# Kernel optimization log

Measured on AMD Instinct MI355X. Metric: run time of the kernel, lower is better.

## Reference

```python
import jax, jax.numpy as jnp
import numpy as np

K = 5  # top-k

def setup_inputs() -> dict:
    key = jax.random.key(0)
    k1, k2, k3 = jax.random.split(key, 3)
    B, L, D = 4096, 100000, 256
    predicted_embeddings = jax.random.normal(k1, (B, D), dtype=jnp.float32)
    label_embeddings = jax.random.normal(k2, (L, D), dtype=jnp.float32)
    true_labels = jax.random.randint(k3, (B,), 0, L, dtype=jnp.int64)
    return {
        "predicted_embeddings": predicted_embeddings,
        "label_embeddings": label_embeddings,
        "true_labels": true_labels,
    }

def reference(predicted_embeddings, label_embeddings, true_labels):
    # (B, L) dense similarity
    similarity = jnp.einsum("bd,ld->bl", predicted_embeddings, label_embeddings)
    _, top_k_indices = jax.lax.top_k(similarity, K)  # (B, K)
    correct = jnp.any(top_k_indices == true_labels[:, None], axis=1)
    accuracy = jnp.mean(correct.astype(jnp.float32))
    return accuracy
```

## Files before the change

### kernel.cpp

```cpp
#include <hip/hip_runtime.h>
#include <hip/hip_bf16.h>

#define B_ROWS   4096
#define L_LABELS 100000
#define D_DIM    256
#define TOPK     5
#define SLABN    64
#define NGROUP   8
#define SLABBYTES 32768

#define CUT       4096
#define NSLAB_C   (CUT / SLABN)
#define NG2       ((L_LABELS - CUT) / 16)
#define P2_BLOCKS 256

typedef __bf16 bf16x8 __attribute__((ext_vector_type(8)));
typedef __bf16 bf16x4 __attribute__((ext_vector_type(4)));
typedef float  f32x4  __attribute__((ext_vector_type(4)));

__device__ __forceinline__ void async16(const void* g, void* l) {
    __builtin_amdgcn_global_load_lds(
        (const __attribute__((address_space(1))) unsigned int*)g,
        (__attribute__((address_space(3))) unsigned int*)l,
        16, 0, 0);
}

__global__ void convertL_kernel(const float* __restrict__ src,
                                __hip_bfloat16* __restrict__ dst) {
    size_t i = ((size_t)blockIdx.x * blockDim.x + threadIdx.x) * 8;
    float4 a = *(const float4*)(src + i);
    float4 b = *(const float4*)(src + i + 4);
    bf16x8 v = {(__bf16)a.x, (__bf16)a.y, (__bf16)a.z, (__bf16)a.w,
                (__bf16)b.x, (__bf16)b.y, (__bf16)b.z, (__bf16)b.w};
    *(bf16x8*)((__bf16*)dst + i) = v;
}

__global__ void prep_kernel(const float* __restrict__ P,
                            const float* __restrict__ Lab,
                            const int*   __restrict__ labels,
                            float* __restrict__ s_t,
                            int*   __restrict__ counts,
                            int*   __restrict__ counts2,
                            __hip_bfloat16* __restrict__ Pb,
                            int do_conv) {
    int gwave = (blockIdx.x * blockDim.x + threadIdx.x) >> 6;
    int lane  = threadIdx.x & 63;
    if (gwave >= B_ROWS) return;
    int t = labels[gwave];
    const float4* p4 = (const float4*)(P + (size_t)gwave * D_DIM);
    const float4* l4 = (const float4*)(Lab + (size_t)t * D_DIM);
    float4 a = p4[lane];
    float4 b = l4[lane];
    if (do_conv) {
        bf16x4 pv = {(__bf16)a.x, (__bf16)a.y, (__bf16)a.z, (__bf16)a.w};
        *(bf16x4*)((__bf16*)Pb + (size_t)gwave * D_DIM + lane * 4) = pv;
    }
    float sum = 0.f;
    sum += (float)(__bf16)a.x * (float)(__bf16)b.x;
    sum += (float)(__bf16)a.y * (float)(__bf16)b.y;
    sum += (float)(__bf16)a.z * (float)(__bf16)b.z;
    sum += (float)(__bf16)a.w * (float)(__bf16)b.w;
    #pragma unroll
    for (int m = 1; m < 64; m <<= 1) sum += __shfl_xor(sum, m, 64);
    if (lane == 0) {
        s_t[gwave]     = sum;
        counts[gwave]  = 0;
        counts2[gwave] = 0;
    }
}

#define CBM 64

__global__ __launch_bounds__(512, 4)
void count_kernel_c1(const __hip_bfloat16* __restrict__ Pb,
                     const __hip_bfloat16* __restrict__ Lb,
                     const int*   __restrict__ labels,
                     const float* __restrict__ s_t,
                     int* __restrict__ counts) {
    __shared__ __align__(16) __bf16 Bs[2 * SLABN * D_DIM];

    const int group = blockIdx.x;
    const int Mbase = blockIdx.y * CBM;
    const int tid   = threadIdx.x;
    const int wave  = tid >> 6;
    const int lane  = tid & 63;
    const int wm    = wave >> 2;
    const int wn    = wave & 3;
    const int quad  = lane >> 4;
    const int cc    = lane & 15;

    const int s0 = group * (NSLAB_C / NGROUP);
    const int s1 = s0 + (NSLAB_C / NGROUP);

    const int qc0  = tid & 31;
    const int rw0  = tid >> 5;
    const int gc0  = (qc0 & 24) | ((qc0 ^ rw0) & 7);
    const int dma0 = rw0 * 512 + gc0 * 16;
    const int ldsw = wave * 1024;

    {
        const char* gbase = (const char*)Lb + (size_t)s0 * SLABBYTES;
        #pragma unroll
        for (int j = 0; j < 4; ++j)
            async16(gbase + dma0 + j * 8192,
                    (char*)Bs + ldsw + j * 8192);
    }

    bf16x8 af[2][8];
    #pragma unroll
    for (int mi = 0; mi < 2; ++mi) {
        int row = Mbase + wm * 32 + mi * 16 + cc;
        const __bf16* ap = (const __bf16*)Pb + (size_t)row * D_DIM + quad * 8;
        #pragma unroll
        for (int kb = 0; kb < 8; ++kb)
            af[mi][kb] = *(const bf16x8*)(ap + kb * 32);
    }

    float sr[2][4];
    int   tr[2][4];
    #pragma unroll
    for (int mi = 0; mi < 2; ++mi)
        #pragma unroll
        for (int r = 0; r < 4; ++r) {
            int row = Mbase + wm * 32 + mi * 16 + quad * 4 + r;
            sr[mi][r] = s_t[row];
            tr[mi][r] = labels[row];
        }

    int cnt[2][4] = {};

    for (int s = s0, it = 0; s < s1; ++s, ++it) {
        __syncthreads();

        if (s + 1 < s1) {
            const char* gbase = (const char*)Lb + (size_t)(s + 1) * SLABBYTES;
            char* lbase = (char*)Bs + (size_t)(~it & 1) * SLABBYTES + ldsw;
            #pragma unroll
            for (int j = 0; j < 4; ++j)
                async16(gbase + dma0 + j * 8192, lbase + j * 8192);
        }

        const __bf16* bp = Bs + (size_t)(it & 1) * (SLABN * D_DIM);

        f32x4 acc[2] = {};
        #pragma unroll
        for (int kb = 0; kb < 8; ++kb) {
            int ci = kb * 4 + quad;
            int qc = (ci & 24) | ((ci ^ cc) & 7);
            bf16x8 b = *(const bf16x8*)&bp[(wn * 16 + cc) * D_DIM + qc * 8];
            #pragma unroll
            for (int mi = 0; mi < 2; ++mi)
                acc[mi] = __builtin_amdgcn_mfma_f32_16x16x32_bf16(
                    af[mi][kb], b, acc[mi], 0, 0, 0);
        }

        int n = s * SLABN + wn * 16 + cc;
        #pragma unroll
        for (int mi = 0; mi < 2; ++mi)
            #pragma unroll
            for (int r = 0; r < 4; ++r) {
                float sv = acc[mi][r];
                bool beat = (n != tr[mi][r]) &&
                            (sv > sr[mi][r] ||
                             (sv == sr[mi][r] && n < tr[mi][r]));
                cnt[mi][r] += beat ? 1 : 0;
            }
    }

    #pragma unroll
    for (int mi = 0; mi < 2; ++mi)
        #pragma unroll
        for (int r = 0; r < 4; ++r) {
            int v = cnt[mi][r];
            v += __shfl_xor(v, 1, 64);
            v += __shfl_xor(v, 2, 64);
            v += __shfl_xor(v, 4, 64);
            v += __shfl_xor(v, 8, 64);
            if (cc == 0) {
                int row = Mbase + wm * 32 + mi * 16 + quad * 4 + r;
                atomicAdd(&counts[row], v);
            }
        }
}

__global__ __launch_bounds__(256)
void count_kernel_p2(const __hip_bfloat16* __restrict__ Pb,
                     const float* __restrict__ Lab,
                     const int*   __restrict__ labels,
                     const float* __restrict__ s_t,
                     const int*   __restrict__ counts,
                     int* __restrict__ counts2) {
    __shared__ int cnt_s[B_ROWS];
    __shared__ int surv_s[B_ROWS];
    __shared__ int ns_s;

    const int tid  = threadIdx.x;
    const int wave = tid >> 6;
    const int lane = tid & 63;
    const int quad = lane >> 4;
    const int cc   = lane & 15;

    #pragma unroll
    for (int i = 0; i < B_ROWS / 256; ++i)
        cnt_s[i * 256 + tid] = counts[i * 256 + tid];
    __syncthreads();

    if (wave == 0) {
        int total = 0;
        for (int base = 0; base < B_ROWS; base += 64) {
            bool sv = cnt_s[base + lane] < TOPK;
            unsigned long long m = __ballot(sv);
            int pos = total + __popcll(m & ((1ull << lane) - 1ull));
            if (sv) surv_s[pos] = base + lane;
            total += __popcll(m);
        }
        if (lane == 0) ns_s = total;
    }
    __syncthreads();

    const int ns = ns_s;
    if (ns == 0) return;
    const int ntiles = (ns + 15) >> 4;

    for (int ti = 0; ti < ntiles; ++ti) {
        int arow = surv_s[min(ti * 16 + cc, ns - 1)];
        bf16x8 af2[8];
        const __bf16* ap = (const __bf16*)Pb + (size_t)arow * D_DIM + quad * 8;
        #pragma unroll
        for (int kb = 0; kb < 8; ++kb)
            af2[kb] = *(const bf16x8*)(ap + kb * 32);

        float sr2[4]; int tr2[4], sidx[4];
        #pragma unroll
        for (int r = 0; r < 4; ++r) {
            int rr  = surv_s[min(ti * 16 + quad * 4 + r, ns - 1)];
            sidx[r] = rr;
            sr2[r]  = s_t[rr];
            tr2[r]  = labels[rr];
        }

        int cnt2[4] = {};
        for (int g = blockIdx.x * 4 + wave; g < NG2; g += P2_BLOCKS * 4) {
            int Lbase = CUT + g * 16;
            const float* bb = Lab + (size_t)(Lbase + cc) * D_DIM + quad * 8;
            f32x4 acc = {};
            #pragma unroll
            for (int kb = 0; kb < 8; ++kb) {
                float4 x = *(const float4*)(bb + kb * 32);
                float4 y = *(const float4*)(bb + kb * 32 + 4);
                bf16x8 b = {(__bf16)x.x, (__bf16)x.y, (__bf16)x.z, (__bf16)x.w,
                            (__bf16)y.x, (__bf16)y.y, (__bf16)y.z, (__bf16)y.w};
                acc = __builtin_amdgcn_mfma_f32_16x16x32_bf16(
                    af2[kb], b, acc, 0, 0, 0);
            }
            int n = Lbase + cc;
            #pragma unroll
            for (int r = 0; r < 4; ++r) {
                float sv = acc[r];
                bool beat = (n != tr2[r]) &&
                            (sv > sr2[r] || (sv == sr2[r] && n < tr2[r]));
                cnt2[r] += beat ? 1 : 0;
            }
        }

        #pragma unroll
        for (int r = 0; r < 4; ++r) {
            int v = cnt2[r];
            v += __shfl_xor(v, 1, 64);
            v += __shfl_xor(v, 2, 64);
            v += __shfl_xor(v, 4, 64);
            v += __shfl_xor(v, 8, 64);
            if (cc == 0 && (ti * 16 + quad * 4 + r) < ns && v)
                atomicAdd(&counts2[sidx[r]], v);
        }
    }
}

#define FBM 128
#define FBN 128
#define FBK 32
#define KPAD 40

__global__ __launch_bounds__(256)
void count_kernel_slow(const float* __restrict__ P,
                       const float* __restrict__ Lab,
                       const int*   __restrict__ labels,
                       const float* __restrict__ s_t,
                       int* __restrict__ counts) {
    __shared__ __align__(16) __bf16 As[FBM][KPAD];
    __shared__ __align__(16) __bf16 Bs[FBN][KPAD];

    const int Nbase = blockIdx.x * FBN;
    const int Mbase = blockIdx.y * FBM;
    const int tid  = threadIdx.x;
    const int lane = tid & 63;
    const int wave = tid >> 6;
    const int wm = wave >> 1;
    const int wn = wave & 1;
    const int quad = lane >> 4;
    const int c    = lane & 15;

    const int srow  = tid >> 1;
    const int skoff = (tid & 1) * 16;
    const int brow_g = min(Nbase + srow, L_LABELS - 1);

    f32x4 acc[4][4] = {};

    for (int Kb = 0; Kb < D_DIM; Kb += FBK) {
        const float* gA = P   + (size_t)(Mbase + srow) * D_DIM + Kb + skoff;
        const float* gB = Lab + (size_t)brow_g        * D_DIM + Kb + skoff;
        #pragma unroll
        for (int i = 0; i < 4; ++i) {
            float4 va = *(const float4*)(gA + i * 4);
            float4 vb = *(const float4*)(gB + i * 4);
            *(bf16x4*)&As[srow][skoff + i * 4] =
                (bf16x4){(__bf16)va.x, (__bf16)va.y, (__bf16)va.z, (__bf16)va.w};
            *(bf16x4*)&Bs[srow][skoff + i * 4] =
                (bf16x4){(__bf16)vb.x, (__bf16)vb.y, (__bf16)vb.z, (__bf16)vb.w};
        }
        __syncthreads();

        bf16x8 afr[4], bfr[4];
        #pragma unroll
        for (int mi = 0; mi < 4; ++mi)
            afr[mi] = *(const bf16x8*)&As[wm * 64 + mi * 16 + c][quad * 8];
        #pragma unroll
        for (int ni = 0; ni < 4; ++ni)
            bfr[ni] = *(const bf16x8*)&Bs[wn * 64 + ni * 16 + c][quad * 8];

        #pragma unroll
        for (int mi = 0; mi < 4; ++mi)
            #pragma unroll
            for (int ni = 0; ni < 4; ++ni)
                acc[mi][ni] = __builtin_amdgcn_mfma_f32_16x16x32_bf16(
                    afr[mi], bfr[ni], acc[mi][ni], 0, 0, 0);
        __syncthreads();
    }

    #pragma unroll
    for (int mi = 0; mi < 4; ++mi) {
        int rowb = Mbase + wm * 64 + mi * 16 + quad * 4;
        #pragma unroll
        for (int r = 0; r < 4; ++r) {
            int   row = rowb + r;
            float st  = s_t[row];
            int   t   = labels[row];
            int   cnt = 0;
            #pragma unroll
            for (int ni = 0; ni < 4; ++ni) {
                int   n = Nbase + wn * 64 + ni * 16 + c;
                float s = acc[mi][ni][r];
                bool beat = (n < L_LABELS) && (n != t) &&
                            (s > st || (s == st && n < t));
                cnt += beat ? 1 : 0;
            }
            cnt += __shfl_xor(cnt, 1, 64);
            cnt += __shfl_xor(cnt, 2, 64);
            cnt += __shfl_xor(cnt, 4, 64);
            cnt += __shfl_xor(cnt, 8, 64);
            if (c == 0 && cnt) atomicAdd(&counts[row], cnt);
        }
    }
}

__global__ void finalize_kernel(const int* __restrict__ counts,
                                const int* __restrict__ counts2,
                                float* __restrict__ out) {
    __shared__ int sdata[4];
    int tid = threadIdx.x;
    int local = 0;
    for (int i = tid; i < B_ROWS; i += 256)
        local += (counts[i] + counts2[i] < TOPK) ? 1 : 0;
    #pragma unroll
    for (int m = 1; m < 64; m <<= 1) local += __shfl_xor(local, m, 64);
    if ((tid & 63) == 0) sdata[tid >> 6] = local;
    __syncthreads();
    if (tid == 0)
        out[0] = (float)(sdata[0] + sdata[1] + sdata[2] + sdata[3]) /
                 (float)B_ROWS;
}

extern "C" void kernel_launch(void* const* d_in, const int* in_sizes, int n_in,
                              void* d_out, int out_size, void* d_ws, size_t ws_size,
                              hipStream_t stream) {
    const float* P      = (const float*)d_in[0];
    const float* Lab    = (const float*)d_in[1];
    const int*   labels = (const int*)d_in[2];
    float* out = (float*)d_out;

    float* s_t     = (float*)d_ws;
    int*   counts  = (int*)((char*)d_ws + 16384);
    int*   counts2 = (int*)((char*)d_ws + 32768);

    const size_t pb_off = 49152;
    const size_t lb_off = pb_off + (size_t)B_ROWS * D_DIM * 2;
    const size_t need   = lb_off + (size_t)CUT * D_DIM * 2;

    int fast = (ws_size >= need) ? 1 : 0;
    __hip_bfloat16* Pb = (__hip_bfloat16*)((char*)d_ws + pb_off);
    __hip_bfloat16* Lb = (__hip_bfloat16*)((char*)d_ws + lb_off);

    prep_kernel<<<dim3(B_ROWS / 4), 256, 0, stream>>>(
        P, Lab, labels, s_t, counts, counts2, Pb, fast);

    if (fast) {
        convertL_kernel<<<dim3((CUT * D_DIM) / 2048), 256, 0, stream>>>(Lab, Lb);
        count_kernel_c1<<<dim3(NGROUP, B_ROWS / CBM), 512, 0, stream>>>(
            Pb, Lb, labels, s_t, counts);
        count_kernel_p2<<<dim3(P2_BLOCKS), 256, 0, stream>>>(
            Pb, Lab, labels, s_t, counts, counts2);
    } else {
        dim3 grid((L_LABELS + FBN - 1) / FBN, B_ROWS / FBM);
        count_kernel_slow<<<grid, 256, 0, stream>>>(P, Lab, labels, s_t, counts);
    }

    finalize_kernel<<<1, 256, 0, stream>>>(counts, counts2, out);
}
```

Before: 209.8 us.

## Fuse label conversion into prep, finalize into pass two, halve cut size

The bf16 conversion of the first label slab moves into the prep kernel, and finalize now runs in the last-finishing block of the pass-two kernel through an atomic done counter. This removes two kernel launches. The exact-pass cut shrinks from 4096 to 2048 labels and pass two gets twice as many blocks. Each pass-two wave now processes two survivor tiles per label load, so the fp32 label reads and their conversion are shared across two MFMAs. The smaller cut may leave more rows surviving pass one, which adds pass-two work, and the two A-fragment sets raise register pressure.

```diff
diff --git a/kernel.cpp b/kernel.cpp
--- a/kernel.cpp
+++ b/kernel.cpp
@@ -9,10 +9,10 @@
 #define NGROUP   8
 #define SLABBYTES 32768
 
-#define CUT       4096
+#define CUT       2048
 #define NSLAB_C   (CUT / SLABN)
 #define NG2       ((L_LABELS - CUT) / 16)
-#define P2_BLOCKS 256
+#define P2_BLOCKS 512
 
 typedef __bf16 bf16x8 __attribute__((ext_vector_type(8)));
 typedef __bf16 bf16x4 __attribute__((ext_vector_type(4)));
@@ -23,16 +23,6 @@
         (const __attribute__((address_space(1))) unsigned int*)g,
         (__attribute__((address_space(3))) unsigned int*)l,
         16, 0, 0);
-}
-
-__global__ void convertL_kernel(const float* __restrict__ src,
-                                __hip_bfloat16* __restrict__ dst) {
-    size_t i = ((size_t)blockIdx.x * blockDim.x + threadIdx.x) * 8;
-    float4 a = *(const float4*)(src + i);
-    float4 b = *(const float4*)(src + i + 4);
-    bf16x8 v = {(__bf16)a.x, (__bf16)a.y, (__bf16)a.z, (__bf16)a.w,
-                (__bf16)b.x, (__bf16)b.y, (__bf16)b.z, (__bf16)b.w};
-    *(bf16x8*)((__bf16*)dst + i) = v;
 }
 
 __global__ void prep_kernel(const float* __restrict__ P,
@@ -42,9 +32,23 @@
                             int*   __restrict__ counts,
                             int*   __restrict__ counts2,
                             __hip_bfloat16* __restrict__ Pb,
+                            __hip_bfloat16* __restrict__ Lb,
+                            int*   __restrict__ done_ctr,
                             int do_conv) {
-    int gwave = (blockIdx.x * blockDim.x + threadIdx.x) >> 6;
-    int lane  = threadIdx.x & 63;
+    int gid = blockIdx.x * blockDim.x + threadIdx.x;
+    if (gid == 0) *done_ctr = 0;
+
+    if (do_conv && gid < (CUT * D_DIM / 8)) {
+        const float* s = Lab + (size_t)gid * 8;
+        float4 a = *(const float4*)s;
+        float4 b = *(const float4*)(s + 4);
+        bf16x8 v = {(__bf16)a.x, (__bf16)a.y, (__bf16)a.z, (__bf16)a.w,
+                    (__bf16)b.x, (__bf16)b.y, (__bf16)b.z, (__bf16)b.w};
+        *(bf16x8*)((__bf16*)Lb + (size_t)gid * 8) = v;
+    }
+
+    int gwave = gid >> 6;
+    int lane  = gid & 63;
     if (gwave >= B_ROWS) return;
     int t = labels[gwave];
     const float4* p4 = (const float4*)(P + (size_t)gwave * D_DIM);
@@ -189,10 +193,13 @@
                      const int*   __restrict__ labels,
                      const float* __restrict__ s_t,
                      const int*   __restrict__ counts,
-                     int* __restrict__ counts2) {
+                     int*   __restrict__ counts2,
+                     int*   __restrict__ done_ctr,
+                     float* __restrict__ out) {
     __shared__ int cnt_s[B_ROWS];
     __shared__ int surv_s[B_ROWS];
-    __shared__ int ns_s;
+    __shared__ int ns_s, rank_s;
+    __shared__ int sred[4];
 
     const int tid  = threadIdx.x;
     const int wave = tid >> 6;
@@ -219,60 +226,95 @@
     __syncthreads();
 
     const int ns = ns_s;
-    if (ns == 0) return;
     const int ntiles = (ns + 15) >> 4;
 
-    for (int ti = 0; ti < ntiles; ++ti) {
-        int arow = surv_s[min(ti * 16 + cc, ns - 1)];
-        bf16x8 af2[8];
-        const __bf16* ap = (const __bf16*)Pb + (size_t)arow * D_DIM + quad * 8;
-        #pragma unroll
-        for (int kb = 0; kb < 8; ++kb)
-            af2[kb] = *(const bf16x8*)(ap + kb * 32);
-
-        float sr2[4]; int tr2[4], sidx[4];
+    for (int ti = 0; ti < ntiles; ti += 2) {
+        const int  tB  = (ti + 1 < ntiles) ? (ti + 1) : ti;
+        const bool dup = (tB == ti);
+
+        int arow0 = surv_s[min(ti * 16 + cc, ns - 1)];
+        int arow1 = surv_s[min(tB * 16 + cc, ns - 1)];
+        bf16x8 af0[8], af1[8];
+        const __bf16* ap0 = (const __bf16*)Pb + (size_t)arow0 * D_DIM + quad * 8;
+        const __bf16* ap1 = (const __bf16*)Pb + (size_t)arow1 * D_DIM + quad * 8;
+        #pragma unroll
+        for (int kb = 0; kb < 8; ++kb) {
+            af0[kb] = *(const bf16x8*)(ap0 + kb * 32);
+            af1[kb] = *(const bf16x8*)(ap1 + kb * 32);
+        }
+
+        float sr2[2][4]; int tr2[2][4], sidx[2][4];
         #pragma unroll
         for (int r = 0; r < 4; ++r) {
-            int rr  = surv_s[min(ti * 16 + quad * 4 + r, ns - 1)];
-            sidx[r] = rr;
-            sr2[r]  = s_t[rr];
-            tr2[r]  = labels[rr];
-        }
-
-        int cnt2[4] = {};
+            int r0 = surv_s[min(ti * 16 + quad * 4 + r, ns - 1)];
+            int r1 = surv_s[min(tB * 16 + quad * 4 + r, ns - 1)];
+            sidx[0][r] = r0;        sidx[1][r] = r1;
+            sr2[0][r]  = s_t[r0];   sr2[1][r]  = s_t[r1];
+            tr2[0][r]  = labels[r0]; tr2[1][r] = labels[r1];
+        }
+
+        int c2a[4] = {}, c2b[4] = {};
         for (int g = blockIdx.x * 4 + wave; g < NG2; g += P2_BLOCKS * 4) {
             int Lbase = CUT + g * 16;
             const float* bb = Lab + (size_t)(Lbase + cc) * D_DIM + quad * 8;
-            f32x4 acc = {};
+            f32x4 acc0 = {}, acc1 = {};
             #pragma unroll
             for (int kb = 0; kb < 8; ++kb) {
                 float4 x = *(const float4*)(bb + kb * 32);
                 float4 y = *(const float4*)(bb + kb * 32 + 4);
                 bf16x8 b = {(__bf16)x.x, (__bf16)x.y, (__bf16)x.z, (__bf16)x.w,
                             (__bf16)y.x, (__bf16)y.y, (__bf16)y.z, (__bf16)y.w};
-                acc = __builtin_amdgcn_mfma_f32_16x16x32_bf16(
-                    af2[kb], b, acc, 0, 0, 0);
+                acc0 = __builtin_amdgcn_mfma_f32_16x16x32_bf16(af0[kb], b, acc0, 0, 0, 0);
+                acc1 = __builtin_amdgcn_mfma_f32_16x16x32_bf16(af1[kb], b, acc1, 0, 0, 0);
             }
             int n = Lbase + cc;
             #pragma unroll
             for (int r = 0; r < 4; ++r) {
-                float sv = acc[r];
-                bool beat = (n != tr2[r]) &&
-                            (sv > sr2[r] || (sv == sr2[r] && n < tr2[r]));
-                cnt2[r] += beat ? 1 : 0;
+                float v0 = acc0[r];
+                c2a[r] += ((n != tr2[0][r]) &&
+                           (v0 > sr2[0][r] || (v0 == sr2[0][r] && n < tr2[0][r]))) ? 1 : 0;
+                float v1 = acc1[r];
+                c2b[r] += ((n != tr2[1][r]) &&
+                           (v1 > sr2[1][r] || (v1 == sr2[1][r] && n < tr2[1][r]))) ? 1 : 0;
             }
         }
 
         #pragma unroll
         for (int r = 0; r < 4; ++r) {
-            int v = cnt2[r];
+            int v = c2a[r];
             v += __shfl_xor(v, 1, 64);
             v += __shfl_xor(v, 2, 64);
             v += __shfl_xor(v, 4, 64);
             v += __shfl_xor(v, 8, 64);
             if (cc == 0 && (ti * 16 + quad * 4 + r) < ns && v)
-                atomicAdd(&counts2[sidx[r]], v);
-        }
+                atomicAdd(&counts2[sidx[0][r]], v);
+            int w = c2b[r];
+            w += __shfl_xor(w, 1, 64);
+            w += __shfl_xor(w, 2, 64);
+            w += __shfl_xor(w, 4, 64);
+            w += __shfl_xor(w, 8, 64);
+            if (cc == 0 && !dup && (tB * 16 + quad * 4 + r) < ns && w)
+                atomicAdd(&counts2[sidx[1][r]], w);
+        }
+    }
+
+    __threadfence();
+    __syncthreads();
+    if (tid == 0) rank_s = atomicAdd(done_ctr, 1);
+    __syncthreads();
+    if (rank_s == P2_BLOCKS - 1) {
+        int local = 0;
+        for (int i = tid; i < B_ROWS; i += 256) {
+            int c2 = atomicAdd(&counts2[i], 0);
+            local += (cnt_s[i] + c2 < TOPK) ? 1 : 0;
+        }
+        #pragma unroll
+        for (int m = 1; m < 64; m <<= 1) local += __shfl_xor(local, m, 64);
+        if ((tid & 63) == 0) sred[tid >> 6] = local;
+        __syncthreads();
+        if (tid == 0)
+            out[0] = (float)(sred[0] + sred[1] + sred[2] + sred[3]) /
+                     (float)B_ROWS;
     }
 }
 
@@ -388,11 +430,12 @@
     const int*   labels = (const int*)d_in[2];
     float* out = (float*)d_out;
 
-    float* s_t     = (float*)d_ws;
-    int*   counts  = (int*)((char*)d_ws + 16384);
-    int*   counts2 = (int*)((char*)d_ws + 32768);
-
-    const size_t pb_off = 49152;
+    float* s_t      = (float*)d_ws;
+    int*   counts   = (int*)((char*)d_ws + 16384);
+    int*   counts2  = (int*)((char*)d_ws + 32768);
+    int*   done_ctr = (int*)((char*)d_ws + 49152);
+
+    const size_t pb_off = 65536;
     const size_t lb_off = pb_off + (size_t)B_ROWS * D_DIM * 2;
     const size_t need   = lb_off + (size_t)CUT * D_DIM * 2;
 
@@ -401,18 +444,16 @@
     __hip_bfloat16* Lb = (__hip_bfloat16*)((char*)d_ws + lb_off);
 
     prep_kernel<<<dim3(B_ROWS / 4), 256, 0, stream>>>(
-        P, Lab, labels, s_t, counts, counts2, Pb, fast);
+        P, Lab, labels, s_t, counts, counts2, Pb, Lb, done_ctr, fast);
 
     if (fast) {
-        convertL_kernel<<<dim3((CUT * D_DIM) / 2048), 256, 0, stream>>>(Lab, Lb);
         count_kernel_c1<<<dim3(NGROUP, B_ROWS / CBM), 512, 0, stream>>>(
             Pb, Lb, labels, s_t, counts);
         count_kernel_p2<<<dim3(P2_BLOCKS), 256, 0, stream>>>(
-            Pb, Lab, labels, s_t, counts, counts2);
+            Pb, Lab, labels, s_t, counts, counts2, done_ctr, out);
     } else {
         dim3 grid((L_LABELS + FBN - 1) / FBN, B_ROWS / FBM);
         count_kernel_slow<<<grid, 256, 0, stream>>>(P, Lab, labels, s_t, counts);
-    }
-
-    finalize_kernel<<<1, 256, 0, stream>>>(counts, counts2, out);
-}
+        finalize_kernel<<<1, 256, 0, stream>>>(counts, counts2, out);
+    }
+}
```

Result: slower. 227.5 us (+8.4%).

## Halve threshold-pass cut, fuse label conversion into prep, compact survivors globally

Applied to the files above, without the earlier changes.

Reduces the first-pass label prefix to 2048 labels. The prefix's bf16 conversion moves into the prep kernel, so the separate conversion launch goes away. Survivor compaction now runs once in a small atomic-based kernel instead of being redone in every phase-2 block through shared memory. A smaller cut means a looser threshold, so more rows may survive into the expensive full-scan phase. Atomic compaction also makes the survivor order nondeterministic.

```diff
diff --git a/kernel.cpp b/kernel.cpp
--- a/kernel.cpp
+++ b/kernel.cpp
@@ -9,7 +9,7 @@
 #define NGROUP   8
 #define SLABBYTES 32768
 
-#define CUT       4096
+#define CUT       2048
 #define NSLAB_C   (CUT / SLABN)
 #define NG2       ((L_LABELS - CUT) / 16)
 #define P2_BLOCKS 256
@@ -23,16 +23,6 @@
         (const __attribute__((address_space(1))) unsigned int*)g,
         (__attribute__((address_space(3))) unsigned int*)l,
         16, 0, 0);
-}
-
-__global__ void convertL_kernel(const float* __restrict__ src,
-                                __hip_bfloat16* __restrict__ dst) {
-    size_t i = ((size_t)blockIdx.x * blockDim.x + threadIdx.x) * 8;
-    float4 a = *(const float4*)(src + i);
-    float4 b = *(const float4*)(src + i + 4);
-    bf16x8 v = {(__bf16)a.x, (__bf16)a.y, (__bf16)a.z, (__bf16)a.w,
-                (__bf16)b.x, (__bf16)b.y, (__bf16)b.z, (__bf16)b.w};
-    *(bf16x8*)((__bf16*)dst + i) = v;
 }
 
 __global__ void prep_kernel(const float* __restrict__ P,
@@ -42,9 +32,23 @@
                             int*   __restrict__ counts,
                             int*   __restrict__ counts2,
                             __hip_bfloat16* __restrict__ Pb,
+                            __hip_bfloat16* __restrict__ Lb,
+                            int*   __restrict__ nsurv,
                             int do_conv) {
-    int gwave = (blockIdx.x * blockDim.x + threadIdx.x) >> 6;
-    int lane  = threadIdx.x & 63;
+    int gid = blockIdx.x * blockDim.x + threadIdx.x;
+    if (gid == 0) *nsurv = 0;
+
+    if (do_conv && gid < (CUT * D_DIM / 8)) {
+        const float* s = Lab + (size_t)gid * 8;
+        float4 a = *(const float4*)s;
+        float4 b = *(const float4*)(s + 4);
+        bf16x8 v = {(__bf16)a.x, (__bf16)a.y, (__bf16)a.z, (__bf16)a.w,
+                    (__bf16)b.x, (__bf16)b.y, (__bf16)b.z, (__bf16)b.w};
+        *(bf16x8*)((__bf16*)Lb + (size_t)gid * 8) = v;
+    }
+
+    int gwave = gid >> 6;
+    int lane  = gid & 63;
     if (gwave >= B_ROWS) return;
     int t = labels[gwave];
     const float4* p4 = (const float4*)(P + (size_t)gwave * D_DIM);
@@ -183,47 +187,36 @@
         }
 }
 
+__global__ void compact_kernel(const int* __restrict__ counts,
+                               int* __restrict__ surv,
+                               int* __restrict__ nsurv) {
+    int row = blockIdx.x * blockDim.x + threadIdx.x;
+    if (row < B_ROWS && counts[row] < TOPK) {
+        int idx = atomicAdd(nsurv, 1);
+        surv[idx] = row;
+    }
+}
+
 __global__ __launch_bounds__(256)
 void count_kernel_p2(const __hip_bfloat16* __restrict__ Pb,
                      const float* __restrict__ Lab,
                      const int*   __restrict__ labels,
                      const float* __restrict__ s_t,
-                     const int*   __restrict__ counts,
+                     const int*   __restrict__ surv,
+                     const int*   __restrict__ nsurv,
                      int* __restrict__ counts2) {
-    __shared__ int cnt_s[B_ROWS];
-    __shared__ int surv_s[B_ROWS];
-    __shared__ int ns_s;
-
     const int tid  = threadIdx.x;
     const int wave = tid >> 6;
     const int lane = tid & 63;
     const int quad = lane >> 4;
     const int cc   = lane & 15;
 
-    #pragma unroll
-    for (int i = 0; i < B_ROWS / 256; ++i)
-        cnt_s[i * 256 + tid] = counts[i * 256 + tid];
-    __syncthreads();
-
-    if (wave == 0) {
-        int total = 0;
-        for (int base = 0; base < B_ROWS; base += 64) {
-            bool sv = cnt_s[base + lane] < TOPK;
-            unsigned long long m = __ballot(sv);
-            int pos = total + __popcll(m & ((1ull << lane) - 1ull));
-            if (sv) surv_s[pos] = base + lane;
-            total += __popcll(m);
-        }
-        if (lane == 0) ns_s = total;
-    }
-    __syncthreads();
-
-    const int ns = ns_s;
+    const int ns = *nsurv;
     if (ns == 0) return;
     const int ntiles = (ns + 15) >> 4;
 
     for (int ti = 0; ti < ntiles; ++ti) {
-        int arow = surv_s[min(ti * 16 + cc, ns - 1)];
+        int arow = surv[min(ti * 16 + cc, ns - 1)];
         bf16x8 af2[8];
         const __bf16* ap = (const __bf16*)Pb + (size_t)arow * D_DIM + quad * 8;
         #pragma unroll
@@ -233,7 +226,7 @@
         float sr2[4]; int tr2[4], sidx[4];
         #pragma unroll
         for (int r = 0; r < 4; ++r) {
-            int rr  = surv_s[min(ti * 16 + quad * 4 + r, ns - 1)];
+            int rr  = surv[min(ti * 16 + quad * 4 + r, ns - 1)];
             sidx[r] = rr;
             sr2[r]  = s_t[rr];
             tr2[r]  = labels[rr];
@@ -391,8 +384,10 @@
     float* s_t     = (float*)d_ws;
     int*   counts  = (int*)((char*)d_ws + 16384);
     int*   counts2 = (int*)((char*)d_ws + 32768);
-
-    const size_t pb_off = 49152;
+    int*   surv    = (int*)((char*)d_ws + 49152);
+    int*   nsurv   = (int*)((char*)d_ws + 65536);
+
+    const size_t pb_off = 69632;
     const size_t lb_off = pb_off + (size_t)B_ROWS * D_DIM * 2;
     const size_t need   = lb_off + (size_t)CUT * D_DIM * 2;
 
@@ -401,14 +396,14 @@
     __hip_bfloat16* Lb = (__hip_bfloat16*)((char*)d_ws + lb_off);
 
     prep_kernel<<<dim3(B_ROWS / 4), 256, 0, stream>>>(
-        P, Lab, labels, s_t, counts, counts2, Pb, fast);
+        P, Lab, labels, s_t, counts, counts2, Pb, Lb, nsurv, fast);
 
     if (fast) {
-        convertL_kernel<<<dim3((CUT * D_DIM) / 2048), 256, 0, stream>>>(Lab, Lb);
         count_kernel_c1<<<dim3(NGROUP, B_ROWS / CBM), 512, 0, stream>>>(
             Pb, Lb, labels, s_t, counts);
+        compact_kernel<<<dim3(B_ROWS / 256), 256, 0, stream>>>(counts, surv, nsurv);
         count_kernel_p2<<<dim3(P2_BLOCKS), 256, 0, stream>>>(
-            Pb, Lab, labels, s_t, counts, counts2);
+            Pb, Lab, labels, s_t, surv, nsurv, counts2);
     } else {
         dim3 grid((L_LABELS + FBN - 1) / FBN, B_ROWS / FBM);
         count_kernel_slow<<<grid, 256, 0, stream>>>(P, Lab, labels, s_t, counts);
```

Measured after the change: 183.6 us. 1.14x faster.
